# Kernel tuning notes

Measured on AMD Instinct MI355X. Metric: run time of the kernel, lower is better.

The kernel has to match this reference:

```python
import jax, jax.numpy as jnp
import numpy as np

N_NODES = 100000
N_EDGES = 1600000
IN_DIM, HID_DIM, OUT_DIM = 128, 128, 64


def setup_inputs() -> dict:
    key = jax.random.key(0)
    k1, k2, k3, k4 = jax.random.split(key, 4)
    x = jax.random.normal(k1, (N_NODES, IN_DIM), dtype=jnp.float32)
    edge_index = jax.random.randint(k2, (2, N_EDGES), 0, N_NODES, dtype=jnp.int32)
    # Glorot-ish init for weights
    W1 = jax.random.normal(k3, (IN_DIM, HID_DIM), dtype=jnp.float32) / np.sqrt(IN_DIM)
    W2 = jax.random.normal(k4, (HID_DIM, OUT_DIM), dtype=jnp.float32) / np.sqrt(HID_DIM)
    b1 = jnp.zeros((HID_DIM,), dtype=jnp.float32)
    b2 = jnp.zeros((OUT_DIM,), dtype=jnp.float32)
    return {"x": x, "edge_index": edge_index, "W1": W1, "b1": b1, "W2": W2, "b2": b2}


def _gcn_norm(edge_index, num_nodes):
    # PyG gcn_norm: add self-loops, symmetric normalization deg^-1/2 A deg^-1/2
    loops = jnp.arange(num_nodes, dtype=edge_index.dtype)
    src = jnp.concatenate([edge_index[0], loops])  # [E+N]
    tgt = jnp.concatenate([edge_index[1], loops])
    deg = jax.ops.segment_sum(jnp.ones_like(tgt, dtype=jnp.float32), tgt,
                              num_segments=num_nodes)
    dinv = jnp.where(deg > 0, jax.lax.rsqrt(deg), 0.0)
    norm = dinv[src] * dinv[tgt]  # [E+N]
    return src, tgt, norm


def _gcn_conv(x, W, b, src, tgt, norm, num_nodes):
    h = x @ W                              # [N, D_out] transform first (GCNConv order)
    msg = norm[:, None] * h[src]           # gather + scale per edge
    agg = jax.ops.segment_sum(msg, tgt, num_segments=num_nodes)  # scatter-add
    return agg + b


def reference(x, edge_index, W1, b1, W2, b2):
    n = x.shape[0]
    src, tgt, norm = _gcn_norm(edge_index, n)
    h = jax.nn.relu(_gcn_conv(x, W1, b1, src, tgt, norm, n))
    out = _gcn_conv(h, W2, b2, src, tgt, norm, n)
    return out
```

## Files before the change

kernel.cpp:

```cpp
#include <hip/hip_runtime.h>


typedef unsigned int uint;
typedef unsigned short ushort;
typedef __attribute__((ext_vector_type(8))) short bf16x8;
typedef __attribute__((ext_vector_type(8))) ushort u16x8;
typedef __attribute__((ext_vector_type(4))) float f32x4;

#define BSHIFT 8
#define MAXBK  512
#define NB     256
#define CAP    8192

__device__ inline ushort f2bf(float f) {
    uint u = __float_as_uint(f);
    return (ushort)((u + 0x7fffu + ((u >> 16) & 1u)) >> 16);
}
__device__ inline float bf_lo(uint u) { return __uint_as_float(u << 16); }
__device__ inline float bf_hi(uint u) { return __uint_as_float(u & 0xffff0000u); }

__global__ __launch_bounds__(256) void hist_kernel(const int* __restrict__ tgt,
                                                   int* __restrict__ counts,
                                                   int E, int chunk, int nbk) {
    __shared__ int hist[MAXBK];
    int t = threadIdx.x, b = blockIdx.x;
    for (int i = t; i < nbk; i += 256) hist[i] = 0;
    __syncthreads();
    int s = b * chunk, e = min(E, s + chunk);
    int i = s + t * 4;
    for (; i + 3 < e; i += 1024) {
        int4 tv = *(const int4*)&tgt[i];
        atomicAdd(&hist[tv.x >> BSHIFT], 1);
        atomicAdd(&hist[tv.y >> BSHIFT], 1);
        atomicAdd(&hist[tv.z >> BSHIFT], 1);
        atomicAdd(&hist[tv.w >> BSHIFT], 1);
    }
    if (i < e)
        for (int k = i; k < e; ++k) atomicAdd(&hist[tgt[k] >> BSHIFT], 1);
    __syncthreads();
    for (int i2 = t; i2 < nbk; i2 += 256) counts[i2 * NB + b] = hist[i2];
}

__global__ __launch_bounds__(256) void scan_partial(const int* __restrict__ in,
                                                    int* __restrict__ bsum, int M) {
    int t = threadIdx.x, b = blockIdx.x;
    int base = b * 1024 + t * 4;
    int s = 0;
#pragma unroll
    for (int k = 0; k < 4; ++k) s += (base + k < M) ? in[base + k] : 0;
#pragma unroll
    for (int off = 32; off > 0; off >>= 1) s += __shfl_down(s, off, 64);
    __shared__ int ws[4];
    if ((t & 63) == 0) ws[t >> 6] = s;
    __syncthreads();
    if (t == 0) bsum[b] = ws[0] + ws[1] + ws[2] + ws[3];
}

__global__ __launch_bounds__(256) void scan_final_counts(int* __restrict__ counts,
                                                         const int* __restrict__ bsum,
                                                         int M) {
    int t = threadIdx.x, b = blockIdx.x;
    int lane = t & 63, wid = t >> 6;
    int p = 0;
    for (int i = t; i < b; i += 256) p += bsum[i];
#pragma unroll
    for (int off = 32; off > 0; off >>= 1) p += __shfl_down(p, off, 64);
    __shared__ int ps[4];
    if (lane == 0) ps[wid] = p;
    __syncthreads();
    int pre = ps[0] + ps[1] + ps[2] + ps[3];

    int base = b * 1024 + t * 4;
    int d[4];
#pragma unroll
    for (int k = 0; k < 4; ++k) d[k] = (base + k < M) ? counts[base + k] : 0;
    int tot = d[0] + d[1] + d[2] + d[3];
    int incl = tot;
#pragma unroll
    for (int off = 1; off < 64; off <<= 1) {
        int u = __shfl_up(incl, off, 64);
        if (lane >= off) incl += u;
    }
    __shared__ int wsum[4];
    if (lane == 63) wsum[wid] = incl;
    __syncthreads();
    int woff = 0;
    for (int w = 0; w < wid; ++w) woff += wsum[w];
    int run = incl - tot + woff + pre;
#pragma unroll
    for (int k = 0; k < 4; ++k) {
        if (base + k < M) counts[base + k] = run;
        run += d[k];
    }
}

__global__ __launch_bounds__(256) void bucket_scatter(const int* __restrict__ src,
                                                      const int* __restrict__ tgt,
                                                      const int* __restrict__ offsets,
                                                      int* __restrict__ tmpP,
                                                      int E, int chunk, int nbk) {
    __shared__ int cur[MAXBK];
    int t = threadIdx.x, b = blockIdx.x;
    for (int i = t; i < nbk; i += 256) cur[i] = offsets[i * NB + b];
    __syncthreads();
    int s = b * chunk, e = min(E, s + chunk);
    int i = s + t * 4;
    for (; i + 3 < e; i += 1024) {
        int4 sv = *(const int4*)&src[i];
        int4 tv = *(const int4*)&tgt[i];
        int p0 = atomicAdd(&cur[tv.x >> BSHIFT], 1);
        tmpP[p0] = (sv.x << BSHIFT) | (tv.x & 255);
        int p1 = atomicAdd(&cur[tv.y >> BSHIFT], 1);
        tmpP[p1] = (sv.y << BSHIFT) | (tv.y & 255);
        int p2 = atomicAdd(&cur[tv.z >> BSHIFT], 1);
        tmpP[p2] = (sv.z << BSHIFT) | (tv.z & 255);
        int p3 = atomicAdd(&cur[tv.w >> BSHIFT], 1);
        tmpP[p3] = (sv.w << BSHIFT) | (tv.w & 255);
    }
    if (i < e) {
        for (int k = i; k < e; ++k) {
            int tg = tgt[k];
            int p = atomicAdd(&cur[tg >> BSHIFT], 1);
            tmpP[p] = (src[k] << BSHIFT) | (tg & 255);
        }
    }
}

__global__ __launch_bounds__(256) void bucket_finish(const int* __restrict__ tmpP,
                                                     const int* __restrict__ offsets,
                                                     int* __restrict__ rowptr,
                                                     float* __restrict__ dinv,
                                                     int* __restrict__ csr_src,
                                                     int N, int E, int nbk) {
    __shared__ int stage[CAP];
    __shared__ int cnt[256];
    __shared__ int wsum[4];
    int t = threadIdx.x, b = blockIdx.x;
    cnt[t] = 0;
    __syncthreads();
    int s = offsets[b * NB];
    int e = (b + 1 < nbk) ? offsets[(b + 1) * NB] : E;
    int m = e - s;
    for (int i = t; i < m; i += 256) {
        int ed = tmpP[s + i];
        if (i < CAP) stage[i] = ed;
        atomicAdd(&cnt[ed & 255], 1);
    }
    __syncthreads();
    int lane = t & 63, wid = t >> 6;
    int d = cnt[t];
    int incl = d;
#pragma unroll
    for (int off = 1; off < 64; off <<= 1) {
        int u = __shfl_up(incl, off, 64);
        if (lane >= off) incl += u;
    }
    if (lane == 63) wsum[wid] = incl;
    __syncthreads();
    int woff = 0;
    for (int w = 0; w < wid; ++w) woff += wsum[w];
    int excl = s + incl - d + woff;
    int node = b * 256 + t;
    if (node < N) {
        rowptr[node] = excl;
        dinv[node] = rsqrtf((float)d + 1.0f);
    }
    if (b == nbk - 1 && t == 255) rowptr[N] = E;
    cnt[t] = excl;
    __syncthreads();
    for (int i = t; i < m; i += 256) {
        int ed = (i < CAP) ? stage[i] : tmpP[s + i];
        int p = atomicAdd(&cnt[ed & 255], 1);
        csr_src[p] = ed >> BSHIFT;
    }
}

template <int M, typename AT>
__global__ __launch_bounds__(256) void gemm_mfma(const AT* __restrict__ A,
                                                 const float* __restrict__ W,
                                                 const float* __restrict__ dinv,
                                                 ushort* __restrict__ C, int N) {
    constexpr int WTS = 136;
    __shared__ ushort WT[M * WTS];
    const int tid = threadIdx.x;
    for (int i = tid; i < 128 * (M / 4); i += 256) {
        int k = i / (M / 4);
        int n0 = (i % (M / 4)) * 4;
        float4 w = *(const float4*)&W[k * M + n0];
        WT[(n0 + 0) * WTS + k] = f2bf(w.x);
        WT[(n0 + 1) * WTS + k] = f2bf(w.y);
        WT[(n0 + 2) * WTS + k] = f2bf(w.z);
        WT[(n0 + 3) * WTS + k] = f2bf(w.w);
    }
    __syncthreads();

    const int wv = tid >> 6, lane = tid & 63;
    const int quad = lane >> 4, mrow = lane & 15;
    int arow_i = blockIdx.x * 64 + wv * 16 + mrow;
    if (arow_i >= N) arow_i = N - 1;
    const AT* arow = &A[(size_t)arow_i * 128];

    f32x4 acc[M / 16];
#pragma unroll
    for (int t = 0; t < M / 16; ++t) acc[t] = (f32x4){0.f, 0.f, 0.f, 0.f};

#pragma unroll
    for (int ks = 0; ks < 4; ++ks) {
        const int k0 = ks * 32 + quad * 8;
        bf16x8 af;
        if constexpr (sizeof(AT) == 4) {
            float4 a0 = *(const float4*)&arow[k0];
            float4 a1 = *(const float4*)&arow[k0 + 4];
            af[0] = (short)f2bf(a0.x); af[1] = (short)f2bf(a0.y);
            af[2] = (short)f2bf(a0.z); af[3] = (short)f2bf(a0.w);
            af[4] = (short)f2bf(a1.x); af[5] = (short)f2bf(a1.y);
            af[6] = (short)f2bf(a1.z); af[7] = (short)f2bf(a1.w);
        } else {
            af = *(const bf16x8*)&arow[k0];
        }
#pragma unroll
        for (int t = 0; t < M / 16; ++t) {
            int n = t * 16 + mrow;
            bf16x8 bfr = *(const bf16x8*)&WT[n * WTS + k0];
            acc[t] = __builtin_amdgcn_mfma_f32_16x16x32_bf16(af, bfr, acc[t], 0, 0, 0);
        }
    }

    const int orow0 = blockIdx.x * 64 + wv * 16 + quad * 4;
#pragma unroll
    for (int r = 0; r < 4; ++r) {
        int orow = orow0 + r;
        if (orow < N) {
            float dv = dinv[orow];
#pragma unroll
            for (int t = 0; t < M / 16; ++t)
                C[(size_t)orow * M + t * 16 + mrow] = f2bf(dv * acc[t][r]);
        }
    }
}

template <int D, bool RELU, bool OUTBF>
__global__ __launch_bounds__(256) void gather_kernel(
    const ushort* __restrict__ h, const int* __restrict__ rowptr,
    const int* __restrict__ csr_src, const float* __restrict__ dinv,
    const float* __restrict__ bias, void* __restrict__ outv, int N) {
    constexpr int Q = D / 8;
    constexpr int G = 64 / Q;
    const int wid = threadIdx.x >> 6, lane = threadIdx.x & 63;
    const int node = blockIdx.x * 4 + wid;
    if (node >= N) return;
    const int g = lane / Q, q = lane % Q;
    const int qoff = q * 8;
    const int beg = rowptr[node], end = rowptr[node + 1];
    float acc[8] = {};

    for (int j = beg; j < end; j += 2 * G) {
        int e0 = j + g, e1 = j + G + g;
        {
            bool v = e0 < end;
            int s = v ? csr_src[e0] : node;
            float m = v ? 1.0f : 0.0f;
            uint4 hv = *(const uint4*)&h[(size_t)s * D + qoff];
            acc[0] += m * bf_lo(hv.x); acc[1] += m * bf_hi(hv.x);
            acc[2] += m * bf_lo(hv.y); acc[3] += m * bf_hi(hv.y);
            acc[4] += m * bf_lo(hv.z); acc[5] += m * bf_hi(hv.z);
            acc[6] += m * bf_lo(hv.w); acc[7] += m * bf_hi(hv.w);
        }
        {
            bool v = e1 < end;
            int s = v ? csr_src[e1] : node;
            float m = v ? 1.0f : 0.0f;
            uint4 hv = *(const uint4*)&h[(size_t)s * D + qoff];
            acc[0] += m * bf_lo(hv.x); acc[1] += m * bf_hi(hv.x);
            acc[2] += m * bf_lo(hv.y); acc[3] += m * bf_hi(hv.y);
            acc[4] += m * bf_lo(hv.z); acc[5] += m * bf_hi(hv.z);
            acc[6] += m * bf_lo(hv.w); acc[7] += m * bf_hi(hv.w);
        }
    }
#pragma unroll
    for (int m2 = Q; m2 < 64; m2 <<= 1)
#pragma unroll
        for (int k = 0; k < 8; ++k) acc[k] += __shfl_xor(acc[k], m2, 64);

    {
        uint4 hv = *(const uint4*)&h[(size_t)node * D + qoff];
        acc[0] += bf_lo(hv.x); acc[1] += bf_hi(hv.x);
        acc[2] += bf_lo(hv.y); acc[3] += bf_hi(hv.y);
        acc[4] += bf_lo(hv.z); acc[5] += bf_hi(hv.z);
        acc[6] += bf_lo(hv.w); acc[7] += bf_hi(hv.w);
    }
    if (g == 0) {
        const float di = dinv[node];
        float4 b0 = *(const float4*)&bias[qoff];
        float4 b1 = *(const float4*)&bias[qoff + 4];
        float r[8] = {di * acc[0] + b0.x, di * acc[1] + b0.y,
                      di * acc[2] + b0.z, di * acc[3] + b0.w,
                      di * acc[4] + b1.x, di * acc[5] + b1.y,
                      di * acc[6] + b1.z, di * acc[7] + b1.w};
        if (RELU) {
#pragma unroll
            for (int k = 0; k < 8; ++k) r[k] = fmaxf(r[k], 0.0f);
        }
        if constexpr (OUTBF) {
            ushort* out = (ushort*)outv;
            u16x8 o;
#pragma unroll
            for (int k = 0; k < 8; ++k) o[k] = f2bf(r[k]);
            *(u16x8*)&out[(size_t)node * D + qoff] = o;
        } else {
            float* out = (float*)outv;
            *(float4*)&out[(size_t)node * D + qoff]     = make_float4(r[0], r[1], r[2], r[3]);
            *(float4*)&out[(size_t)node * D + qoff + 4] = make_float4(r[4], r[5], r[6], r[7]);
        }
    }
}

extern "C" void kernel_launch(void* const* d_in, const int* in_sizes, int n_in,
                              void* d_out, int out_size, void* d_ws, size_t ws_size,
                              hipStream_t stream) {
    const float* x  = (const float*)d_in[0];
    const int*   ei = (const int*)d_in[1];
    const float* W1 = (const float*)d_in[2];
    const float* b1 = (const float*)d_in[3];
    const float* W2 = (const float*)d_in[4];
    const float* b2 = (const float*)d_in[5];
    float* out = (float*)d_out;

    const int N = in_sizes[0] / 128;
    const int E = in_sizes[1] / 2;
    const int* src = ei;
    const int* tgt = ei + E;

    const int nbk   = (N + 255) >> BSHIFT;
    const int chunk = (((E + NB - 1) / NB) + 3) & ~3;
    const int Mc    = nbk * NB;

    float* ws = (float*)d_ws;
    const size_t Np = (size_t)((N + 3) & ~3);
    float*  dinv    = ws;
    int*    rowptr  = (int*)(ws + Np);
    int*    counts  = rowptr + Np + 4;
    int*    bsum    = counts + MAXBK * NB;
    int*    csr_src = bsum + 128;
    int*    tmpP    = csr_src + E;
    ushort* h       = (ushort*)(tmpP + E);
    ushort* h1      = h + (size_t)N * 128;
    ushort* h2      = h;

    const int nbc = (Mc + 1023) / 1024;

    hist_kernel<<<NB, 256, 0, stream>>>(tgt, counts, E, chunk, nbk);
    scan_partial<<<nbc, 256, 0, stream>>>(counts, bsum, Mc);
    scan_final_counts<<<nbc, 256, 0, stream>>>(counts, bsum, Mc);
    bucket_scatter<<<NB, 256, 0, stream>>>(src, tgt, counts, tmpP, E, chunk, nbk);
    bucket_finish<<<nbk, 256, 0, stream>>>(tmpP, counts, rowptr, dinv, csr_src, N, E, nbk);

    gemm_mfma<128, float><<<(N + 63) / 64, 256, 0, stream>>>(x, W1, dinv, h, N);
    gather_kernel<128, true, true><<<(N + 3) / 4, 256, 0, stream>>>(
        h, rowptr, csr_src, dinv, b1, h1, N);

    gemm_mfma<64, ushort><<<(N + 63) / 64, 256, 0, stream>>>(h1, W2, dinv, h2, N);
    gather_kernel<64, false, false><<<(N + 3) / 4, 256, 0, stream>>>(
        h2, rowptr, csr_src, dinv, b2, out, N);
}
```

Baseline: 310.5 us.

## Slice node features into column panels so gathers hit cache per slice

The GEMM epilogue now writes its output as eight column slices laid out contiguously. A new gather kernel processes one slice per block and walks 8 nodes per wave. The idea is that each slice's feature table is small enough to stay cache-resident during the random neighbor gathers. In exchange, the CSR index and rowptr reads are repeated once per slice, gather loads become narrow (16–32 bytes), and lane utilization drops.

```diff
diff --git a/kernel.cpp b/kernel.cpp
--- a/kernel.cpp
+++ b/kernel.cpp
@@ -175,7 +175,7 @@
     }
 }
 
-template <int M, typename AT>
+template <int M, int SCOLS, typename AT>
 __global__ __launch_bounds__(256) void gemm_mfma(const AT* __restrict__ A,
                                                  const float* __restrict__ W,
                                                  const float* __restrict__ dinv,
@@ -233,84 +233,83 @@
         if (orow < N) {
             float dv = dinv[orow];
 #pragma unroll
-            for (int t = 0; t < M / 16; ++t)
-                C[(size_t)orow * M + t * 16 + mrow] = f2bf(dv * acc[t][r]);
-        }
-    }
-}
-
-template <int D, bool RELU, bool OUTBF>
-__global__ __launch_bounds__(256) void gather_kernel(
-    const ushort* __restrict__ h, const int* __restrict__ rowptr,
+            for (int t = 0; t < M / 16; ++t) {
+                int col = t * 16 + mrow;
+                int slice = col / SCOLS, within = col % SCOLS;
+                C[(size_t)slice * N * SCOLS + (size_t)orow * SCOLS + within] =
+                    f2bf(dv * acc[t][r]);
+            }
+        }
+    }
+}
+
+template <int COLS, bool RELU, bool OUTBF, int OS>
+__global__ __launch_bounds__(256) void gather_sliced(
+    const ushort* __restrict__ hbase, const int* __restrict__ rowptr,
     const int* __restrict__ csr_src, const float* __restrict__ dinv,
     const float* __restrict__ bias, void* __restrict__ outv, int N) {
-    constexpr int Q = D / 8;
+    constexpr int Q = COLS / 8;
     constexpr int G = 64 / Q;
+    const int slice = blockIdx.x & 7;
+    const int group = blockIdx.x >> 3;
     const int wid = threadIdx.x >> 6, lane = threadIdx.x & 63;
-    const int node = blockIdx.x * 4 + wid;
-    if (node >= N) return;
     const int g = lane / Q, q = lane % Q;
     const int qoff = q * 8;
-    const int beg = rowptr[node], end = rowptr[node + 1];
-    float acc[8] = {};
-
-    for (int j = beg; j < end; j += 2 * G) {
-        int e0 = j + g, e1 = j + G + g;
-        {
-            bool v = e0 < end;
-            int s = v ? csr_src[e0] : node;
+    const ushort* __restrict__ h = hbase + (size_t)slice * N * COLS;
+    const float* bs = bias + slice * COLS;
+    const int cbase = slice * COLS + qoff;
+
+    for (int i = 0; i < 8; ++i) {
+        int node = group * 32 + wid * 8 + i;
+        if (node >= N) break;
+        const int beg = rowptr[node], end = rowptr[node + 1];
+        float acc[8] = {};
+        for (int j = beg; j < end; j += G) {
+            int e = j + g;
+            bool v = e < end;
+            int s = v ? csr_src[e] : node;
             float m = v ? 1.0f : 0.0f;
-            uint4 hv = *(const uint4*)&h[(size_t)s * D + qoff];
+            uint4 hv = *(const uint4*)&h[(size_t)s * COLS + qoff];
             acc[0] += m * bf_lo(hv.x); acc[1] += m * bf_hi(hv.x);
             acc[2] += m * bf_lo(hv.y); acc[3] += m * bf_hi(hv.y);
             acc[4] += m * bf_lo(hv.z); acc[5] += m * bf_hi(hv.z);
             acc[6] += m * bf_lo(hv.w); acc[7] += m * bf_hi(hv.w);
         }
+#pragma unroll
+        for (int mk = Q; mk < 64; mk <<= 1)
+#pragma unroll
+            for (int k = 0; k < 8; ++k) acc[k] += __shfl_xor(acc[k], mk, 64);
+
         {
-            bool v = e1 < end;
-            int s = v ? csr_src[e1] : node;
-            float m = v ? 1.0f : 0.0f;
-            uint4 hv = *(const uint4*)&h[(size_t)s * D + qoff];
-            acc[0] += m * bf_lo(hv.x); acc[1] += m * bf_hi(hv.x);
-            acc[2] += m * bf_lo(hv.y); acc[3] += m * bf_hi(hv.y);
-            acc[4] += m * bf_lo(hv.z); acc[5] += m * bf_hi(hv.z);
-            acc[6] += m * bf_lo(hv.w); acc[7] += m * bf_hi(hv.w);
-        }
-    }
-#pragma unroll
-    for (int m2 = Q; m2 < 64; m2 <<= 1)
-#pragma unroll
-        for (int k = 0; k < 8; ++k) acc[k] += __shfl_xor(acc[k], m2, 64);
-
-    {
-        uint4 hv = *(const uint4*)&h[(size_t)node * D + qoff];
-        acc[0] += bf_lo(hv.x); acc[1] += bf_hi(hv.x);
-        acc[2] += bf_lo(hv.y); acc[3] += bf_hi(hv.y);
-        acc[4] += bf_lo(hv.z); acc[5] += bf_hi(hv.z);
-        acc[6] += bf_lo(hv.w); acc[7] += bf_hi(hv.w);
-    }
-    if (g == 0) {
-        const float di = dinv[node];
-        float4 b0 = *(const float4*)&bias[qoff];
-        float4 b1 = *(const float4*)&bias[qoff + 4];
-        float r[8] = {di * acc[0] + b0.x, di * acc[1] + b0.y,
-                      di * acc[2] + b0.z, di * acc[3] + b0.w,
-                      di * acc[4] + b1.x, di * acc[5] + b1.y,
-                      di * acc[6] + b1.z, di * acc[7] + b1.w};
-        if (RELU) {
-#pragma unroll
-            for (int k = 0; k < 8; ++k) r[k] = fmaxf(r[k], 0.0f);
-        }
-        if constexpr (OUTBF) {
-            ushort* out = (ushort*)outv;
-            u16x8 o;
-#pragma unroll
-            for (int k = 0; k < 8; ++k) o[k] = f2bf(r[k]);
-            *(u16x8*)&out[(size_t)node * D + qoff] = o;
-        } else {
-            float* out = (float*)outv;
-            *(float4*)&out[(size_t)node * D + qoff]     = make_float4(r[0], r[1], r[2], r[3]);
-            *(float4*)&out[(size_t)node * D + qoff + 4] = make_float4(r[4], r[5], r[6], r[7]);
+            uint4 hv = *(const uint4*)&h[(size_t)node * COLS + qoff];
+            acc[0] += bf_lo(hv.x); acc[1] += bf_hi(hv.x);
+            acc[2] += bf_lo(hv.y); acc[3] += bf_hi(hv.y);
+            acc[4] += bf_lo(hv.z); acc[5] += bf_hi(hv.z);
+            acc[6] += bf_lo(hv.w); acc[7] += bf_hi(hv.w);
+        }
+        if (g == 0) {
+            const float di = dinv[node];
+            float4 b0 = *(const float4*)&bs[qoff];
+            float4 b1 = *(const float4*)&bs[qoff + 4];
+            float r[8] = {di * acc[0] + b0.x, di * acc[1] + b0.y,
+                          di * acc[2] + b0.z, di * acc[3] + b0.w,
+                          di * acc[4] + b1.x, di * acc[5] + b1.y,
+                          di * acc[6] + b1.z, di * acc[7] + b1.w};
+            if (RELU) {
+#pragma unroll
+                for (int k = 0; k < 8; ++k) r[k] = fmaxf(r[k], 0.0f);
+            }
+            if constexpr (OUTBF) {
+                ushort* out = (ushort*)outv;
+                u16x8 o;
+#pragma unroll
+                for (int k = 0; k < 8; ++k) o[k] = f2bf(r[k]);
+                *(u16x8*)&out[(size_t)node * OS + cbase] = o;
+            } else {
+                float* out = (float*)outv;
+                *(float4*)&out[(size_t)node * OS + cbase]     = make_float4(r[0], r[1], r[2], r[3]);
+                *(float4*)&out[(size_t)node * OS + cbase + 4] = make_float4(r[4], r[5], r[6], r[7]);
+            }
         }
     }
 }
@@ -348,6 +347,7 @@
     ushort* h2      = h;
 
     const int nbc = (Mc + 1023) / 1024;
+    const int ngrp = (N + 31) / 32;
 
     hist_kernel<<<NB, 256, 0, stream>>>(tgt, counts, E, chunk, nbk);
     scan_partial<<<nbc, 256, 0, stream>>>(counts, bsum, Mc);
@@ -355,11 +355,11 @@
     bucket_scatter<<<NB, 256, 0, stream>>>(src, tgt, counts, tmpP, E, chunk, nbk);
     bucket_finish<<<nbk, 256, 0, stream>>>(tmpP, counts, rowptr, dinv, csr_src, N, E, nbk);
 
-    gemm_mfma<128, float><<<(N + 63) / 64, 256, 0, stream>>>(x, W1, dinv, h, N);
-    gather_kernel<128, true, true><<<(N + 3) / 4, 256, 0, stream>>>(
+    gemm_mfma<128, 16, float><<<(N + 63) / 64, 256, 0, stream>>>(x, W1, dinv, h, N);
+    gather_sliced<16, true, true, 128><<<ngrp * 8, 256, 0, stream>>>(
         h, rowptr, csr_src, dinv, b1, h1, N);
 
-    gemm_mfma<64, ushort><<<(N + 63) / 64, 256, 0, stream>>>(h1, W2, dinv, h2, N);
-    gather_kernel<64, false, false><<<(N + 3) / 4, 256, 0, stream>>>(
+    gemm_mfma<64, 8, ushort><<<(N + 63) / 64, 256, 0, stream>>>(h1, W2, dinv, h2, N);
+    gather_sliced<8, false, false, 64><<<ngrp * 8, 256, 0, stream>>>(
         h2, rowptr, csr_src, dinv, b2, out, N);
 }
```

Result: slower. 893.7 us (+187.8%).
